# Kernel tuning notes

Measured on AMD Instinct MI355X. Metric: run time of the kernel, lower is better.

Reference implementation:

```python
import jax, jax.numpy as jnp
import numpy as np

N = 100000   # total nodes across all graphs
E = 1600000  # edges (avg degree 16)
D = 128      # input feature dim
H = 64       # hidden dim
B = 8        # number of graphs
EPS = 1e-5   # BatchNorm eps


def setup_inputs() -> dict:
    key = jax.random.key(0)
    ks = jax.random.split(key, 12)
    x = jax.random.normal(ks[0], (N, D), dtype=jnp.float32)
    edge_index = jax.random.randint(ks[1], (2, E), 0, N, dtype=jnp.int64)
    batch = jnp.sort(jax.random.randint(ks[2], (N,), 0, B, dtype=jnp.int64))
    s1 = 1.0 / np.sqrt(D)
    s2 = 1.0 / np.sqrt(H)
    W1l = jax.random.uniform(ks[3], (D, H), minval=-s1, maxval=s1, dtype=jnp.float32)
    W1r = jax.random.uniform(ks[4], (D, H), minval=-s1, maxval=s1, dtype=jnp.float32)
    b1 = jnp.zeros((H,), jnp.float32)
    gamma1 = jnp.ones((H,), jnp.float32)
    beta1 = jnp.zeros((H,), jnp.float32)
    W2l = jax.random.uniform(ks[5], (H, H), minval=-s2, maxval=s2, dtype=jnp.float32)
    W2r = jax.random.uniform(ks[6], (H, H), minval=-s2, maxval=s2, dtype=jnp.float32)
    b2 = jnp.zeros((H,), jnp.float32)
    return {"x": x, "edge_index": edge_index, "batch": batch,
            "W1l": W1l, "b1": b1, "W1r": W1r, "gamma1": gamma1, "beta1": beta1,
            "W2l": W2l, "b2": b2, "W2r": W2r}


def _seg_mean(vals, idx, num):
    # scatter-mean: sum per segment / count, zero-degree segments give 0 (count clamped)
    s = jax.ops.segment_sum(vals, idx, num_segments=num)
    cnt = jax.ops.segment_sum(jnp.ones((idx.shape[0], 1), vals.dtype), idx, num_segments=num)
    return s / jnp.maximum(cnt, 1.0)


def reference(x, edge_index, batch, W1l, b1, W1r, gamma1, beta1, W2l, b2, W2r):
    src, dst = edge_index[0], edge_index[1]
    # SAGEConv layer 1: mean-aggregate neighbors, lin_l(agg) + lin_r(x)
    agg1 = _seg_mean(x[src], dst, N)            # [N, D]
    h = agg1 @ W1l + b1 + x @ W1r               # [N, H]
    # BatchNorm1d (training-mode batch stats, biased var) then ReLU
    mu = jnp.mean(h, axis=0)
    var = jnp.var(h, axis=0)
    h = (h - mu) * jax.lax.rsqrt(var + EPS) * gamma1 + beta1
    h = jax.nn.relu(h)
    # SAGEConv layer 2 (no norm/act after last layer)
    agg2 = _seg_mean(h[src], dst, N)            # [N, H]
    h2 = agg2 @ W2l + b2 + h @ W2r              # [N, H]
    # per-graph global mean pool -> [B, H]
    return _seg_mean(h2, batch, B)
```

## Files before the change

kernel.cpp:

```cpp
#include <hip/hip_runtime.h>

#define N_NODES 100000
#define E_EDGES 1600000
#define DIM 128
#define HID 64
#define NGRAPH 8
#define EPSBN 1e-5f

#define GSHIFT 9
#define GNODES (1 << GSHIFT)
#define NGROUP ((N_NODES + GNODES - 1) >> GSHIFT)
#define GCAP 10240
#define CHUNK 2048
#define PBLK 256
#define EPT (CHUNK / PBLK)
#define NCHUNK ((E_EDGES + CHUNK - 1) / CHUNK)
#define MM1B ((N_NODES + 63) / 64)
#define GATB 2048

#if __has_builtin(__builtin_amdgcn_cvt_pk_fp8_f32) && \
    __has_builtin(__builtin_amdgcn_cvt_pk_f32_fp8)
#define HW_FP8 1
#else
#define HW_FP8 0
#endif

typedef float floatx2 __attribute__((ext_vector_type(2)));

__device__ __forceinline__ unsigned f2bf_pack(float lo, float hi) {
  unsigned ul = __float_as_uint(lo);
  unsigned uh = __float_as_uint(hi);
  ul = (ul + 0x7fffu + ((ul >> 16) & 1u)) >> 16;
  uh = (uh + 0x7fffu + ((uh >> 16) & 1u)) >> 16;
  return (uh << 16) | ul;
}
__device__ __forceinline__ float bflo(unsigned u) {
  return __uint_as_float(u << 16);
}
__device__ __forceinline__ float bfhi(unsigned u) {
  return __uint_as_float(u & 0xffff0000u);
}

#if !HW_FP8
__device__ __forceinline__ unsigned char f32_to_e4m3(float f) {
  unsigned u = __float_as_uint(f);
  unsigned s = (u >> 24) & 0x80u;
  float a = fabsf(f);
  if (a >= 464.f) return (unsigned char)(s | 0x7E);
  if (a < 0.015625f) {
    int m = (int)rintf(a * 512.f);
    if (m >= 8) return (unsigned char)(s | 0x08);
    return (unsigned char)(s | (unsigned)m);
  }
  int e = (int)((u >> 23) & 0xFF) - 127;
  float q = ldexpf(a, -e) * 8.f;
  int m = (int)rintf(q);
  if (m == 16) { m = 8; ++e; }
  if (e > 8) return (unsigned char)(s | 0x7E);
  return (unsigned char)(s | (unsigned)(((e + 7) << 3) | (m - 8)));
}
#endif

__device__ __forceinline__ unsigned pack4_e4m3(float a, float b, float c,
                                               float d) {
#if HW_FP8
  int w = __builtin_amdgcn_cvt_pk_fp8_f32(a, b, 0, false);
  w = __builtin_amdgcn_cvt_pk_fp8_f32(c, d, w, true);
  return (unsigned)w;
#else
  return (unsigned)f32_to_e4m3(a) | ((unsigned)f32_to_e4m3(b) << 8) |
         ((unsigned)f32_to_e4m3(c) << 16) | ((unsigned)f32_to_e4m3(d) << 24);
#endif
}

__global__ __launch_bounds__(PBLK) void part_mm1_kernel(
    const int* __restrict__ src, const int* __restrict__ dst,
    int* __restrict__ gcnt, unsigned* __restrict__ part,
    const float* __restrict__ x, const float* __restrict__ W1l,
    const float* __restrict__ W1r, unsigned char* __restrict__ y1f8,
    unsigned* __restrict__ y2bf) {
  __shared__ int hist[256];
  __shared__ int sc[256];
  __shared__ int scanoff[256];
  __shared__ int gbase[256];
  __shared__ unsigned buf[CHUNK];
  __shared__ unsigned char gid[CHUNK];

  if (blockIdx.x < NCHUNK) {
    int c = blockIdx.x;
    int e0 = c * CHUNK;
    int m = E_EDGES - e0;
    m = m < CHUNK ? m : CHUNK;
    int t = threadIdx.x;

    hist[t] = 0;
    __syncthreads();

    int myg[EPT];
    unsigned mytok[EPT];
    int myrank[EPT];
    #pragma unroll
    for (int q = 0; q < EPT; ++q) {
      int i = t + q * PBLK;
      if (i < m) {
        int d = dst[e0 + i];
        int s = src[e0 + i];
        int g = d >> GSHIFT;
        myg[q] = g;
        mytok[q] = ((unsigned)(d & (GNODES - 1)) << 17) | (unsigned)s;
        myrank[q] = atomicAdd(&hist[g], 1);
      } else {
        myg[q] = -1;
      }
    }
    __syncthreads();

    sc[t] = hist[t];
    if (t < NGROUP && hist[t] > 0) gbase[t] = atomicAdd(&gcnt[t], hist[t]);
    __syncthreads();
    for (int off = 1; off < 256; off <<= 1) {
      int add = (t >= off) ? sc[t - off] : 0;
      __syncthreads();
      sc[t] += add;
      __syncthreads();
    }
    scanoff[t] = sc[t] - hist[t];
    __syncthreads();

    #pragma unroll
    for (int q = 0; q < EPT; ++q) {
      if (myg[q] >= 0) {
        int pos = scanoff[myg[q]] + myrank[q];
        buf[pos] = mytok[q];
        gid[pos] = (unsigned char)myg[q];
      }
    }
    __syncthreads();

    for (int i = t; i < m; i += PBLK) {
      int g = gid[i];
      int addr = gbase[g] + (i - scanoff[g]);
      if (addr < GCAP) part[(size_t)g * GCAP + addr] = buf[i];
    }
  } else {
    int lane = threadIdx.x & 63;
    int c0 = __builtin_amdgcn_readfirstlane((int)(threadIdx.x >> 6) << 4);
    int n = (blockIdx.x - NCHUNK) * 64 + lane;
    if (n >= N_NODES) return;
    const float* xr = x + (size_t)n * DIM;

    float a1[16], a2[16];
    #pragma unroll
    for (int j = 0; j < 16; ++j) { a1[j] = 0.f; a2[j] = 0.f; }

    for (int k = 0; k < DIM; k += 4) {
      float4 xv = *reinterpret_cast<const float4*>(xr + k);
      float xs[4] = {xv.x, xv.y, xv.z, xv.w};
      #pragma unroll
      for (int kk = 0; kk < 4; ++kk) {
        const float* w1 = W1l + (size_t)(k + kk) * HID + c0;
        const float* w2 = W1r + (size_t)(k + kk) * HID + c0;
        float xk = xs[kk];
        #pragma unroll
        for (int j = 0; j < 16; ++j) {
          a1[j] = fmaf(xk, w1[j], a1[j]);
          a2[j] = fmaf(xk, w2[j], a2[j]);
        }
      }
    }
    uint4 pk;
    pk.x = pack4_e4m3(a1[0], a1[1], a1[2], a1[3]);
    pk.y = pack4_e4m3(a1[4], a1[5], a1[6], a1[7]);
    pk.z = pack4_e4m3(a1[8], a1[9], a1[10], a1[11]);
    pk.w = pack4_e4m3(a1[12], a1[13], a1[14], a1[15]);
    *reinterpret_cast<uint4*>(y1f8 + (size_t)n * HID + c0) = pk;

    uint4 q0, q1;
    q0.x = f2bf_pack(a2[0], a2[1]);
    q0.y = f2bf_pack(a2[2], a2[3]);
    q0.z = f2bf_pack(a2[4], a2[5]);
    q0.w = f2bf_pack(a2[6], a2[7]);
    q1.x = f2bf_pack(a2[8], a2[9]);
    q1.y = f2bf_pack(a2[10], a2[11]);
    q1.z = f2bf_pack(a2[12], a2[13]);
    q1.w = f2bf_pack(a2[14], a2[15]);
    unsigned* ob = y2bf + (size_t)n * (HID / 2) + (c0 >> 1);
    reinterpret_cast<uint4*>(ob)[0] = q0;
    reinterpret_cast<uint4*>(ob)[1] = q1;
  }
}

__global__ __launch_bounds__(512) void groupcsr_kernel(
    const int* __restrict__ gcnt, const unsigned* __restrict__ part,
    const int* __restrict__ batch, int* __restrict__ rowptr,
    int* __restrict__ csr, unsigned* __restrict__ tok2) {
  __shared__ int hist[GNODES];
  __shared__ int excl[GNODES];
  __shared__ int degl[GNODES];
  __shared__ int batl[GNODES];
  __shared__ int sc2[256];
  int g = blockIdx.x;
  int t = threadIdx.x;

  if (t < 256) sc2[t] = (t < NGROUP) ? min(gcnt[t], GCAP) : 0;
  __syncthreads();
  for (int off = 1; off < 256; off <<= 1) {
    int add = (t < 256 && t >= off) ? sc2[t - off] : 0;
    __syncthreads();
    if (t < 256) sc2[t] += add;
    __syncthreads();
  }
  int gbase = (g > 0) ? sc2[g - 1] : 0;

  hist[t] = 0;
  {
    int n = (g << GSHIFT) + t;
    batl[t] = (n < N_NODES) ? batch[n] : 0;
  }
  __syncthreads();

  int cnt = min(gcnt[g], GCAP);
  const unsigned* ga = part + (size_t)g * GCAP;
  for (int i = t; i < cnt; i += 512) atomicAdd(&hist[ga[i] >> 17], 1);
  __syncthreads();

  int orig = hist[t];
  degl[t] = orig;
  for (int off = 1; off < GNODES; off <<= 1) {
    int add = (t >= off) ? hist[t - off] : 0;
    __syncthreads();
    hist[t] += add;
    __syncthreads();
  }
  excl[t] = hist[t] - orig;
  __syncthreads();

  int n = (g << GSHIFT) + t;
  if (n <= N_NODES) rowptr[n] = gbase + excl[t];
  if (g == 0 && t == 0) rowptr[0] = 0;
  __syncthreads();

  for (int i = t; i < cnt; i += 512) {
    unsigned p = ga[i];
    int dloc = (int)(p >> 17);
    int pos = gbase + atomicAdd(&excl[dloc], 1);
    unsigned s = p & 0x1FFFFu;
    csr[pos] = (int)s;
    unsigned dg = (unsigned)degl[dloc];
    if (dg > 1023u) dg = 1023u;
    tok2[pos] = (dg << 20) | ((unsigned)batl[dloc] << 17) | s;
  }
}

__global__ __launch_bounds__(PBLK) void part2_gather_kernel(
    const unsigned* __restrict__ tok2, int* __restrict__ gcnt2,
    unsigned* __restrict__ part2, const uint2* __restrict__ yf8,
    const int* __restrict__ csr, const int* __restrict__ rowptr,
    const unsigned* __restrict__ otherbf, const float* __restrict__ bias,
    float* __restrict__ outC, float* __restrict__ stats) {
  __shared__ int hist[256];
  __shared__ int sc[256];
  __shared__ int scanoff[256];
  __shared__ int gbase[256];
  __shared__ unsigned buf[CHUNK];
  __shared__ unsigned char gid[CHUNK];
  __shared__ float ss[HID];
  __shared__ float sq[HID];

  if (blockIdx.x < NCHUNK) {
    int c = blockIdx.x;
    int e0 = c * CHUNK;
    int m = E_EDGES - e0;
    m = m < CHUNK ? m : CHUNK;
    int t = threadIdx.x;

    hist[t] = 0;
    __syncthreads();

    int myg[EPT];
    unsigned mytok[EPT];
    int myrank[EPT];
    #pragma unroll
    for (int q = 0; q < EPT; ++q) {
      int i = t + q * PBLK;
      if (i < m) {
        unsigned p = tok2[e0 + i];
        int g = (int)((p & 0x1FFFFu) >> GSHIFT);
        myg[q] = g;
        mytok[q] = p;
        myrank[q] = atomicAdd(&hist[g], 1);
      } else {
        myg[q] = -1;
      }
    }
    __syncthreads();

    sc[t] = hist[t];
    if (t < NGROUP && hist[t] > 0) gbase[t] = atomicAdd(&gcnt2[t], hist[t]);
    __syncthreads();
    for (int off = 1; off < 256; off <<= 1) {
      int add = (t >= off) ? sc[t - off] : 0;
      __syncthreads();
      sc[t] += add;
      __syncthreads();
    }
    scanoff[t] = sc[t] - hist[t];
    __syncthreads();

    #pragma unroll
    for (int q = 0; q < EPT; ++q) {
      if (myg[q] >= 0) {
        int pos = scanoff[myg[q]] + myrank[q];
        buf[pos] = mytok[q];
        gid[pos] = (unsigned char)myg[q];
      }
    }
    __syncthreads();

    for (int i = t; i < m; i += PBLK) {
      int g = gid[i];
      int addr = gbase[g] + (i - scanoff[g]);
      if (addr < GCAP) part2[(size_t)g * GCAP + addr] = buf[i];
    }
  } else {
#if !HW_FP8
    __shared__ float tbl[256];
    {
      int t = threadIdx.x;
      if (t < 256) {
        int e = (t >> 3) & 15;
        int m = t & 7;
        float v = e ? ldexpf((float)(8 + m), e - 10) : ldexpf((float)m, -9);
        tbl[t] = (t & 0x80) ? -v : v;
      }
    }
    __syncthreads();
#endif
    int lane = threadIdx.x & 63;
    int oct = lane >> 3;
    int lo = lane & 7;
    int gbid = blockIdx.x - NCHUNK;
    int wid = (gbid * PBLK + (int)threadIdx.x) >> 6;
    const int nw = (GATB * PBLK) >> 6;

    float bj[8];
    #pragma unroll
    for (int k = 0; k < 8; ++k) bj[k] = bias[lo * 8 + k];

    float ls[8], lq[8];
    #pragma unroll
    for (int k = 0; k < 8; ++k) { ls[k] = 0.f; lq[k] = 0.f; }

    for (int nb = wid * 8; nb < N_NODES; nb += nw * 8) {
      int n = nb + oct;
      bool valid = n < N_NODES;
      int start = valid ? rowptr[n] : 0;
      int end = valid ? rowptr[n + 1] : 0;

      float acc[8];
      #pragma unroll
      for (int k = 0; k < 8; ++k) acc[k] = 0.f;

      for (int bse = start; bse < end; bse += 8) {
        int m = end - bse;
        m = m < 8 ? m : 8;
        int e = bse + lo;
        int s = (e < end) ? csr[e] : 0;
        uint2 vv[8];
        #pragma unroll
        for (int i = 0; i < 8; ++i) {
          int si = __shfl(s, i, 8);
          vv[i] = yf8[(size_t)si * 8 + lo];
        }
        #pragma unroll
        for (int i = 0; i < 8; ++i) {
          if (i < m) {
#if HW_FP8
            floatx2 p0 = __builtin_amdgcn_cvt_pk_f32_fp8((int)vv[i].x, false);
            floatx2 p1 = __builtin_amdgcn_cvt_pk_f32_fp8((int)vv[i].x, true);
            floatx2 p2 = __builtin_amdgcn_cvt_pk_f32_fp8((int)vv[i].y, false);
            floatx2 p3 = __builtin_amdgcn_cvt_pk_f32_fp8((int)vv[i].y, true);
            acc[0] += p0[0];
            acc[1] += p0[1];
            acc[2] += p1[0];
            acc[3] += p1[1];
            acc[4] += p2[0];
            acc[5] += p2[1];
            acc[6] += p3[0];
            acc[7] += p3[1];
#else
            acc[0] += tbl[vv[i].x & 255u];
            acc[1] += tbl[(vv[i].x >> 8) & 255u];
            acc[2] += tbl[(vv[i].x >> 16) & 255u];
            acc[3] += tbl[vv[i].x >> 24];
            acc[4] += tbl[vv[i].y & 255u];
            acc[5] += tbl[(vv[i].y >> 8) & 255u];
            acc[6] += tbl[(vv[i].y >> 16) & 255u];
            acc[7] += tbl[vv[i].y >> 24];
#endif
          }
        }
      }

      if (valid) {
        int deg = end - start;
        float inv = 1.f / (float)(deg > 1 ? deg : 1);
        uint4 ov = *reinterpret_cast<const uint4*>(otherbf +
                                                   (size_t)n * (HID / 2) +
                                                   lo * 4);
        float v[8];
        v[0] = fmaf(acc[0], inv, bj[0]) + bflo(ov.x);
        v[1] = fmaf(acc[1], inv, bj[1]) + bfhi(ov.x);
        v[2] = fmaf(acc[2], inv, bj[2]) + bflo(ov.y);
        v[3] = fmaf(acc[3], inv, bj[3]) + bfhi(ov.y);
        v[4] = fmaf(acc[4], inv, bj[4]) + bflo(ov.z);
        v[5] = fmaf(acc[5], inv, bj[5]) + bfhi(ov.z);
        v[6] = fmaf(acc[6], inv, bj[6]) + bflo(ov.w);
        v[7] = fmaf(acc[7], inv, bj[7]) + bfhi(ov.w);
        float* wp = outC + (size_t)n * HID + lo * 8;
        *reinterpret_cast<float4*>(wp) = make_float4(v[0], v[1], v[2], v[3]);
        *reinterpret_cast<float4*>(wp + 4) =
            make_float4(v[4], v[5], v[6], v[7]);
        #pragma unroll
        for (int k = 0; k < 8; ++k) {
          ls[k] += v[k];
          lq[k] = fmaf(v[k], v[k], lq[k]);
        }
      }
    }

    int t = threadIdx.x;
    if (t < HID) { ss[t] = 0.f; sq[t] = 0.f; }
    __syncthreads();
    #pragma unroll
    for (int k = 0; k < 8; ++k) {
      atomicAdd(&ss[lo * 8 + k], ls[k]);
      atomicAdd(&sq[lo * 8 + k], lq[k]);
    }
    __syncthreads();
    if (t < HID) {
      unsafeAtomicAdd(&stats[t], ss[t]);
      unsafeAtomicAdd(&stats[HID + t], sq[t]);
    }
  }
}

__global__ __launch_bounds__(256) void chsum_kernel(
    const int* __restrict__ gcnt2, const unsigned* __restrict__ part2,
    const float* __restrict__ Cc, const float* __restrict__ stats,
    const float* __restrict__ gamma, const float* __restrict__ beta,
    const int* __restrict__ batch, float* __restrict__ S1g,
    float* __restrict__ S2g) {
  __shared__ float c[GNODES * NGRAPH];
  __shared__ float r1[HID * NGRAPH];
  __shared__ float r2[HID * NGRAPH];
  int g = blockIdx.x;
  int t = threadIdx.x;

  for (int i = t; i < GNODES * NGRAPH; i += 256) c[i] = 0.f;
  for (int i = t; i < HID * NGRAPH; i += 256) { r1[i] = 0.f; r2[i] = 0.f; }
  __syncthreads();

  int cnt = min(gcnt2[g], GCAP);
  const unsigned* ga = part2 + (size_t)g * GCAP;
  for (int i = t; i < cnt; i += 256) {
    unsigned p = ga[i];
    int sl = (int)(p & (GNODES - 1));
    int b = (int)((p >> 17) & 7u);
    int deg = (int)((p >> 20) & 0x3FFu);
    float w = 1.f / (float)(deg > 1 ? deg : 1);
    atomicAdd(&c[sl * NGRAPH + b], w);
  }
  __syncthreads();

  int lane = t & 63;
  int wv = t >> 6;

  float inv_n = 1.0f / (float)N_NODES;
  float mu = stats[lane] * inv_n;
  float var = stats[HID + lane] * inv_n - mu * mu;
  float scl = gamma[lane] * rsqrtf(var + EPSBN);
  float shf = beta[lane] - mu * scl;

  float s1[NGRAPH], s2[NGRAPH];
  #pragma unroll
  for (int b = 0; b < NGRAPH; ++b) { s1[b] = 0.f; s2[b] = 0.f; }

  int nend = N_NODES - (g << GSHIFT);
  nend = nend < GNODES ? nend : GNODES;
  for (int nl = wv; nl < nend; nl += 4) {
    int n = (g << GSHIFT) + nl;
    float hr = Cc[(size_t)n * HID + lane];
    float h = fmaf(hr, scl, shf);
    h = h > 0.f ? h : 0.f;
    int bn = batch[n];
    #pragma unroll
    for (int b = 0; b < NGRAPH; ++b) {
      float cb = c[nl * NGRAPH + b];
      s1[b] = fmaf(cb, h, s1[b]);
      s2[b] += (b == bn) ? h : 0.f;
    }
  }

  #pragma unroll
  for (int b = 0; b < NGRAPH; ++b) {
    atomicAdd(&r1[b * HID + lane], s1[b]);
    atomicAdd(&r2[b * HID + lane], s2[b]);
  }
  __syncthreads();
  for (int i = t; i < HID * NGRAPH; i += 256) {
    unsafeAtomicAdd(&S1g[i], r1[i]);
    unsafeAtomicAdd(&S2g[i], r2[i]);
  }
}

__device__ __forceinline__ int lbound(const int* __restrict__ a, int key) {
  int lo = 0, hi = N_NODES;
  while (lo < hi) {
    int mid = (lo + hi) >> 1;
    if (a[mid] < key) lo = mid + 1; else hi = mid;
  }
  return lo;
}

__global__ __launch_bounds__(512) void finale_kernel(
    const float* __restrict__ S1g, const float* __restrict__ S2g,
    const int* __restrict__ batch, const float* __restrict__ W2l,
    const float* __restrict__ W2r, const float* __restrict__ b2,
    float* __restrict__ out) {
  int t = threadIdx.x;
  int b = t >> 6;
  int oc = t & 63;
  int V = lbound(batch, b + 1) - lbound(batch, b);
  float acc = 0.f;
  for (int k = 0; k < HID; ++k) {
    acc = fmaf(S1g[b * HID + k], W2l[k * HID + oc], acc);
    acc = fmaf(S2g[b * HID + k], W2r[k * HID + oc], acc);
  }
  out[t] = (V > 0) ? (acc / (float)V + b2[oc]) : 0.f;
}

extern "C" void kernel_launch(void* const* d_in, const int* in_sizes, int n_in,
                              void* d_out, int out_size, void* d_ws,
                              size_t ws_size, hipStream_t stream) {
  const float* x      = (const float*)d_in[0];
  const int*   ei     = (const int*)d_in[1];
  const int*   batch  = (const int*)d_in[2];
  const float* W1l    = (const float*)d_in[3];
  const float* b1     = (const float*)d_in[4];
  const float* W1r    = (const float*)d_in[5];
  const float* gamma1 = (const float*)d_in[6];
  const float* beta1  = (const float*)d_in[7];
  const float* W2l    = (const float*)d_in[8];
  const float* b2     = (const float*)d_in[9];
  const float* W2r    = (const float*)d_in[10];

  const int* src = ei;
  const int* dst = ei + E_EDGES;

  float* ws = (float*)d_ws;
  size_t off = 0;
  unsigned char* Af8 = (unsigned char*)(ws + off);
  off += (size_t)N_NODES * HID / 4;
  unsigned* Bbf = (unsigned*)(ws + off);
  off += (size_t)N_NODES * (HID / 2);
  float* Cc = ws + off; off += (size_t)N_NODES * HID;
  int* gcnt     = (int*)(ws + off); off += 256;
  int* gcnt2    = (int*)(ws + off); off += 256;
  float* stats  = ws + off; off += 2 * HID;
  float* S1g    = ws + off; off += NGRAPH * HID;
  float* S2g    = ws + off; off += NGRAPH * HID;
  size_t zero_elems = 256 + 256 + 2 * HID + 2 * NGRAPH * HID;
  int* rowptr   = (int*)(ws + off); off += N_NODES + 1;
  int* csr      = (int*)(ws + off); off += E_EDGES;
  unsigned* tok2 = (unsigned*)(ws + off); off += E_EDGES;
  unsigned* part = (unsigned*)(ws + off); off += (size_t)NGROUP * GCAP;

  hipMemsetAsync(gcnt, 0, zero_elems * sizeof(float), stream);

  part_mm1_kernel<<<NCHUNK + MM1B, PBLK, 0, stream>>>(
      src, dst, gcnt, part, x, W1l, W1r, Af8, Bbf);

  groupcsr_kernel<<<NGROUP, 512, 0, stream>>>(gcnt, part, batch, rowptr, csr,
                                              tok2);

  part2_gather_kernel<<<NCHUNK + GATB, PBLK, 0, stream>>>(
      tok2, gcnt2, part, (const uint2*)Af8, csr, rowptr, Bbf, b1, Cc, stats);

  chsum_kernel<<<NGROUP, 256, 0, stream>>>(gcnt2, part, Cc, stats, gamma1,
                                           beta1, batch, S1g, S2g);

  finale_kernel<<<1, 512, 0, stream>>>(S1g, S2g, batch, W2l, W2r, b2,
                                       (float*)d_out);
}
```

Measured before the change: 263.5 us.

## Stage x tile in swizzled LDS for mm1 and store pre-BN activations as bf16

The node-matmul branch of the first kernel now loads a 64-row tile of x into shared memory with coalesced float4 loads and an XOR swizzle. Each lane then reads its row from LDS instead of issuing strided global loads per lane. Separately, the pre-BatchNorm layer-1 output is written as packed bf16 instead of fp32, halving the write in the gather kernel and the read in chsum. BN statistics are still accumulated from the fp32 values, but the normalized activations now come from bf16-rounded data, which adds precision loss.

```diff
diff --git a/kernel.cpp b/kernel.cpp
--- a/kernel.cpp
+++ b/kernel.cpp
@@ -79,14 +79,16 @@
     const float* __restrict__ x, const float* __restrict__ W1l,
     const float* __restrict__ W1r, unsigned char* __restrict__ y1f8,
     unsigned* __restrict__ y2bf) {
-  __shared__ int hist[256];
-  __shared__ int sc[256];
-  __shared__ int scanoff[256];
-  __shared__ int gbase[256];
-  __shared__ unsigned buf[CHUNK];
-  __shared__ unsigned char gid[CHUNK];
+  __shared__ __align__(16) unsigned char smraw[32768];
 
   if (blockIdx.x < NCHUNK) {
+    int* hist = (int*)(smraw);
+    int* sc = (int*)(smraw + 1024);
+    int* scanoff = (int*)(smraw + 2048);
+    int* gbase = (int*)(smraw + 3072);
+    unsigned* buf = (unsigned*)(smraw + 4096);
+    unsigned char* gid = smraw + 12288;
+
     int c = blockIdx.x;
     int e0 = c * CHUNK;
     int m = E_EDGES - e0;
@@ -143,18 +145,35 @@
       if (addr < GCAP) part[(size_t)g * GCAP + addr] = buf[i];
     }
   } else {
-    int lane = threadIdx.x & 63;
-    int c0 = __builtin_amdgcn_readfirstlane((int)(threadIdx.x >> 6) << 4);
-    int n = (blockIdx.x - NCHUNK) * 64 + lane;
+    float* xlds = (float*)smraw;
+    int t = threadIdx.x;
+    int brow = (blockIdx.x - NCHUNK) * 64;
+
+    for (int i = t; i < 64 * 32; i += PBLK) {
+      int r = i >> 5;
+      int c4 = (i & 31) << 2;
+      int n = brow + r;
+      if (n < N_NODES) {
+        float4 v = *reinterpret_cast<const float4*>(x + (size_t)n * DIM + c4);
+        int w = c4 ^ ((r & 7) << 2);
+        *reinterpret_cast<float4*>(xlds + r * DIM + w) = v;
+      }
+    }
+    __syncthreads();
+
+    int lane = t & 63;
+    int c0 = __builtin_amdgcn_readfirstlane((int)(t >> 6) << 4);
+    int n = brow + lane;
     if (n >= N_NODES) return;
-    const float* xr = x + (size_t)n * DIM;
+    const float* xr = xlds + lane * DIM;
+    int sw = (lane & 7) << 2;
 
     float a1[16], a2[16];
     #pragma unroll
     for (int j = 0; j < 16; ++j) { a1[j] = 0.f; a2[j] = 0.f; }
 
     for (int k = 0; k < DIM; k += 4) {
-      float4 xv = *reinterpret_cast<const float4*>(xr + k);
+      float4 xv = *reinterpret_cast<const float4*>(xr + (k ^ sw));
       float xs[4] = {xv.x, xv.y, xv.z, xv.w};
       #pragma unroll
       for (int kk = 0; kk < 4; ++kk) {
@@ -257,7 +276,7 @@
     unsigned* __restrict__ part2, const uint2* __restrict__ yf8,
     const int* __restrict__ csr, const int* __restrict__ rowptr,
     const unsigned* __restrict__ otherbf, const float* __restrict__ bias,
-    float* __restrict__ outC, float* __restrict__ stats) {
+    unsigned* __restrict__ outCbf, float* __restrict__ stats) {
   __shared__ int hist[256];
   __shared__ int sc[256];
   __shared__ int scanoff[256];
@@ -417,10 +436,13 @@
         v[5] = fmaf(acc[5], inv, bj[5]) + bfhi(ov.z);
         v[6] = fmaf(acc[6], inv, bj[6]) + bflo(ov.w);
         v[7] = fmaf(acc[7], inv, bj[7]) + bfhi(ov.w);
-        float* wp = outC + (size_t)n * HID + lo * 8;
-        *reinterpret_cast<float4*>(wp) = make_float4(v[0], v[1], v[2], v[3]);
-        *reinterpret_cast<float4*>(wp + 4) =
-            make_float4(v[4], v[5], v[6], v[7]);
+        uint4 cw4;
+        cw4.x = f2bf_pack(v[0], v[1]);
+        cw4.y = f2bf_pack(v[2], v[3]);
+        cw4.z = f2bf_pack(v[4], v[5]);
+        cw4.w = f2bf_pack(v[6], v[7]);
+        *reinterpret_cast<uint4*>(outCbf + (size_t)n * (HID / 2) + lo * 4) =
+            cw4;
         #pragma unroll
         for (int k = 0; k < 8; ++k) {
           ls[k] += v[k];
@@ -447,7 +469,7 @@
 
 __global__ __launch_bounds__(256) void chsum_kernel(
     const int* __restrict__ gcnt2, const unsigned* __restrict__ part2,
-    const float* __restrict__ Cc, const float* __restrict__ stats,
+    const unsigned* __restrict__ Cbf, const float* __restrict__ stats,
     const float* __restrict__ gamma, const float* __restrict__ beta,
     const int* __restrict__ batch, float* __restrict__ S1g,
     float* __restrict__ S2g) {
@@ -490,7 +512,8 @@
   nend = nend < GNODES ? nend : GNODES;
   for (int nl = wv; nl < nend; nl += 4) {
     int n = (g << GSHIFT) + nl;
-    float hr = Cc[(size_t)n * HID + lane];
+    unsigned u = Cbf[(size_t)n * (HID / 2) + (lane >> 1)];
+    float hr = (lane & 1) ? bfhi(u) : bflo(u);
     float h = fmaf(hr, scl, shf);
     h = h > 0.f ? h : 0.f;
     int bn = batch[n];
@@ -564,7 +587,8 @@
   off += (size_t)N_NODES * HID / 4;
   unsigned* Bbf = (unsigned*)(ws + off);
   off += (size_t)N_NODES * (HID / 2);
-  float* Cc = ws + off; off += (size_t)N_NODES * HID;
+  unsigned* Cbf = (unsigned*)(ws + off);
+  off += (size_t)N_NODES * (HID / 2);
   int* gcnt     = (int*)(ws + off); off += 256;
   int* gcnt2    = (int*)(ws + off); off += 256;
   float* stats  = ws + off; off += 2 * HID;
@@ -585,9 +609,9 @@
                                               tok2);
 
   part2_gather_kernel<<<NCHUNK + GATB, PBLK, 0, stream>>>(
-      tok2, gcnt2, part, (const uint2*)Af8, csr, rowptr, Bbf, b1, Cc, stats);
-
-  chsum_kernel<<<NGROUP, 256, 0, stream>>>(gcnt2, part, Cc, stats, gamma1,
+      tok2, gcnt2, part, (const uint2*)Af8, csr, rowptr, Bbf, b1, Cbf, stats);
+
+  chsum_kernel<<<NGROUP, 256, 0, stream>>>(gcnt2, part, Cbf, stats, gamma1,
                                            beta1, batch, S1g, S2g);
 
   finale_kernel<<<1, 512, 0, stream>>>(S1g, S2g, batch, W2l, W2r, b2,
```

Result: slower. 272.7 us (+3.5%).
